# Kernel optimization log

Hardware: AMD Instinct MI355X
Metric: run time of the kernel (lower is better)

## Reference

```python
import jax, jax.numpy as jnp
import numpy as np
from jax import lax

B, C, T = 512, 63, 250          # batch, EEG channels, timepoints
S = 10                           # number of subjects
E = 4                            # emb_size of CNN projection
HID, PROJ = 184, 1024            # hidden_dim (=4*46), embed_dim
EPS = 1e-5
DN = ('NCHW', 'OIHW', 'NCHW')


def setup_inputs() -> dict:
    key = jax.random.key(0)
    ks = jax.random.split(key, 16)
    p = {}
    p['x'] = jax.random.normal(ks[0], (B, C, T), dtype=jnp.float32)
    p['subjects'] = jax.random.randint(ks[1], (B,), 0, S, dtype=jnp.int32)
    # per-subject Linear(T, T): weight [S, T, T], bias [S, T]
    p['W_subj'] = jax.random.normal(ks[2], (S, T, T), dtype=jnp.float32) * 0.02
    p['b_subj'] = jnp.zeros((S, T), dtype=jnp.float32)
    # tsconv
    p['conv1_w'] = jax.random.normal(ks[3], (40, 1, 1, 5), dtype=jnp.float32) * 0.1
    p['conv1_b'] = jnp.zeros((40,), dtype=jnp.float32)
    p['bn1_g'] = jnp.ones((40,), dtype=jnp.float32)
    p['bn1_b'] = jnp.zeros((40,), dtype=jnp.float32)
    p['conv2_w'] = jax.random.normal(ks[4], (40, 40, C, 1), dtype=jnp.float32) * 0.02
    p['conv2_b'] = jnp.zeros((40,), dtype=jnp.float32)
    p['bn2_g'] = jnp.ones((40,), dtype=jnp.float32)
    p['bn2_b'] = jnp.zeros((40,), dtype=jnp.float32)
    # 1x1 projection conv to emb_size
    p['proj_w'] = jax.random.normal(ks[5], (E, 40, 1, 1), dtype=jnp.float32) * 0.1
    p['proj_b'] = jnp.zeros((E,), dtype=jnp.float32)
    # MLP projector
    p['fc1_w'] = jax.random.normal(ks[6], (PROJ, HID), dtype=jnp.float32) * 0.05
    p['fc1_b'] = jnp.zeros((PROJ,), dtype=jnp.float32)
    p['fc2_w'] = jax.random.normal(ks[7], (PROJ, PROJ), dtype=jnp.float32) * 0.02
    p['fc2_b'] = jnp.zeros((PROJ,), dtype=jnp.float32)
    p['ln_g'] = jnp.ones((PROJ,), dtype=jnp.float32)
    p['ln_b'] = jnp.zeros((PROJ,), dtype=jnp.float32)
    return p


def _bn(h, g, b):
    # BatchNorm2d with batch statistics over (N, H, W), NCHW layout
    mu = jnp.mean(h, axis=(0, 2, 3), keepdims=True)
    var = jnp.var(h, axis=(0, 2, 3), keepdims=True)
    return (h - mu) * lax.rsqrt(var + EPS) * g[None, :, None, None] + b[None, :, None, None]


def _avgpool_w(h, k, s):
    # average pool over last (W) dim, kernel k stride s
    summed = lax.reduce_window(h, 0.0, lax.add, (1, 1, 1, k), (1, 1, 1, s), 'VALID')
    return summed / k


def reference(x, subjects, W_subj, b_subj, conv1_w, conv1_b, bn1_g, bn1_b,
              conv2_w, conv2_b, bn2_g, bn2_b, proj_w, proj_b,
              fc1_w, fc1_b, fc2_w, fc2_b, ln_g, ln_b):
    # --- subject-conditioned linear dispatch (grouped GEMM via gather) ---
    Wg = W_subj[subjects]                      # [B, T, T]
    bg = b_subj[subjects]                      # [B, T]
    x_eeg = jnp.einsum('bct,bst->bcs', x, Wg) + bg[:, None, :]   # [B, C, T]

    # --- Spatio_Temporal_CNN ---
    h = x_eeg[:, None, :, :]                   # [B, 1, C, T]
    h = lax.conv_general_dilated(h, conv1_w, (1, 1), 'VALID', dimension_numbers=DN)
    h = h + conv1_b[None, :, None, None]       # [B, 40, C, 246]
    h = _avgpool_w(h, 17, 5)                   # [B, 40, C, 46]
    h = jax.nn.elu(_bn(h, bn1_g, bn1_b))
    h = lax.conv_general_dilated(h, conv2_w, (1, 1), 'VALID', dimension_numbers=DN)
    h = h + conv2_b[None, :, None, None]       # [B, 40, 1, 46]
    h = jax.nn.elu(_bn(h, bn2_g, bn2_b))       # dropout = identity (eval)
    h = lax.conv_general_dilated(h, proj_w, (1, 1), 'VALID', dimension_numbers=DN)
    h = h + proj_b[None, :, None, None]        # [B, E, 1, 46]
    # Rearrange 'b e h w -> b (h w) e' then flatten -> [B, 46*E] = [B, 184]
    z = jnp.transpose(h, (0, 2, 3, 1)).reshape(h.shape[0], -1)

    # --- MLP projector ---
    h1 = z @ fc1_w.T + fc1_b                   # [B, 1024]
    r = jax.nn.gelu(h1, approximate=False) @ fc2_w.T + fc2_b
    h2 = h1 + r                                # ResidualAdd (dropout = identity)
    mu = jnp.mean(h2, axis=-1, keepdims=True)
    var = jnp.var(h2, axis=-1, keepdims=True)
    return (h2 - mu) * lax.rsqrt(var + EPS) * ln_g + ln_b
```

## Files before the change

### kernel.cpp

```cpp
#include <hip/hip_runtime.h>
#include <hip/hip_bf16.h>

#define K2 2520
#define PROJ 1024
#define HID 184
#define N1F (512.f*63.f*46.f)
#define N2F (512.f*46.f)

typedef float f32x4 __attribute__((ext_vector_type(4)));
typedef short bf16x8 __attribute__((ext_vector_type(8)));
typedef unsigned short u16;
typedef unsigned short ushort8 __attribute__((ext_vector_type(8)));
typedef unsigned int u32;
typedef unsigned int u32x2 __attribute__((ext_vector_type(2)));
typedef unsigned int u32x4 __attribute__((ext_vector_type(4)));

__device__ __forceinline__ u16 f2bf(float f) {
    unsigned u = __builtin_bit_cast(unsigned, f);
    return (u16)((u + 0x7FFFu + ((u >> 16) & 1u)) >> 16);
}
__device__ __forceinline__ float bf2f(u16 h) {
    unsigned u = ((unsigned)h) << 16;
    return __builtin_bit_cast(float, u);
}
__device__ __forceinline__ u32 cvtpk(float lo, float hi) {
    u32 r;
    asm("v_cvt_pk_bf16_f32 %0, %1, %2" : "=v"(r) : "v"(lo), "v"(hi));
    return r;
}

__global__ void kX(const float* __restrict__ W, const float* __restrict__ w2,
                   const float* __restrict__ fw1, const float* __restrict__ fw2,
                   u16* __restrict__ Wbf, u16* __restrict__ Wbf2,
                   u16* __restrict__ fwbf1, u16* __restrict__ fwbf2, float* stats) {
    int bid = blockIdx.x, tid = threadIdx.x;
    if (bid == 0 && tid < 320) stats[tid] = 0.f;
    if (bid < 2560) {
        int i = bid*256 + tid;
        int j  = i & 7, kg = (i >> 3) & 3, row = (i >> 5) & 15;
        int nf = (i >> 9) & 15, ks = (i >> 13) & 7, sj = i >> 16;
        int s_ = nf*16 + row, t_ = ks*32 + kg*8 + j;
        float v = (s_ < 250 && t_ < 250) ? W[(size_t)sj*62500 + s_*250 + t_] : 0.f;
        Wbf[i] = f2bf(v);
    } else if (bid < 3034) {
        int i = (bid-2560)*256 + tid;
        int n = i / 2528, k = i - n*2528;
        float v = 0.f;
        if (n < 40 && k < K2) { int c = k/40, o = k - c*40; v = w2[n*K2 + o*63 + c]; }
        Wbf2[i] = f2bf(v);
    } else if (bid < 3802) {
        int i = (bid-3034)*256 + tid;
        int n = i/192, k = i - n*192;
        fwbf1[i] = f2bf(k < HID ? fw1[n*HID + k] : 0.f);
    } else {
        int i = (bid-3802)*256 + tid;
        fwbf2[i] = f2bf(fw2[i]);
    }
}

#define XS(c,s) xs[(c)*258 + (s)]
__global__ __launch_bounds__(256) void kAB(const float* __restrict__ x,
                                           const int* __restrict__ subj,
                                           const u16* __restrict__ Wpk,
                                           const float* __restrict__ bsub,
                                           const float* __restrict__ w1,
                                           const float* __restrict__ b1,
                                           u16* __restrict__ pooled,
                                           float* __restrict__ stats) {
    __shared__ float xs[32*258 + 16];
    __shared__ u16 effh[48*32] __attribute__((aligned(16)));
    __shared__ u16 effl[48*32] __attribute__((aligned(16)));
    __shared__ float biasL[256];
    __shared__ float sS[4][48], sQ[4][48];
    int b = blockIdx.x, ch = blockIdx.y;
    int sj = subj[b];
    int tid = threadIdx.x;
    int wv = tid >> 6, lane = tid & 63, row = lane & 15, kg = lane >> 4;

    {
        int srow = tid >> 3, st8 = tid & 7;
        int cg0 = ch*32 + srow;
        const float* xrow = x + ((size_t)b*63 + (cg0 < 63 ? cg0 : 62))*250;
        #pragma unroll
        for (int q = 0; q < 16; ++q) {
            int c2i = st8 + 8*q;
            if (c2i < 125) {
                float2 v = *(const float2*)&xrow[2*c2i];
                *(float2*)&XS(srow, 2*c2i) = v;
            }
        }
        XS(srow, 250 + st8) = 0.f;
        if (tid < 16) xs[32*258 + tid] = 0.f;
    }
    biasL[tid] = (tid < 250) ? bsub[sj*250 + tid] : 0.f;
    for (int i = tid; i < 1536; i += 256) {
        int o = i >> 5, tap = i & 31;
        float e = 0.f;
        if (o < 40 && tap < 21) {
            #pragma unroll
            for (int k = 0; k < 5; ++k) { int u = tap - k; if (u >= 0 && u <= 16) e += w1[o*5+k]; }
            e *= (1.f/17.f);
        }
        u16 h = f2bf(e);
        effh[i] = h;
        effl[i] = f2bf(e - bf2f(h));
    }
    __syncthreads();

    int cgrp = wv & 1, nfh = wv >> 1;
    const u16* Wp = Wpk + (size_t)sj*65536 + ((size_t)row*4 + kg)*8;
    f32x4 acc[8];
    #pragma unroll
    for (int i = 0; i < 8; ++i) acc[i] = (f32x4){0.f,0.f,0.f,0.f};
    #pragma unroll
    for (int ks = 0; ks < 8; ++ks) {
        int tb = ks*32 + kg*8;
        float av[8];
        #pragma unroll
        for (int j = 0; j < 8; ++j) av[j] = XS(cgrp*16 + row, tb + j);
        u32x4 p;
        p[0]=cvtpk(av[0],av[1]); p[1]=cvtpk(av[2],av[3]);
        p[2]=cvtpk(av[4],av[5]); p[3]=cvtpk(av[6],av[7]);
        bf16x8 af = __builtin_bit_cast(bf16x8, p);
        #pragma unroll
        for (int nf2 = 0; nf2 < 8; ++nf2) {
            bf16x8 bv = *(const bf16x8*)(Wp + (size_t)(ks*16 + nfh*8 + nf2)*512);
            acc[nf2] = __builtin_amdgcn_mfma_f32_16x16x32_bf16(af, bv, acc[nf2], 0, 0, 0);
        }
    }
    __syncthreads();
    int cw = cgrp*16 + kg*4;
    #pragma unroll
    for (int nf2 = 0; nf2 < 8; ++nf2) {
        int s = (nfh*8 + nf2)*16 + row;
        float bias = biasL[s];
        #pragma unroll
        for (int r = 0; r < 4; ++r) XS(cw + r, s) = acc[nf2][r] + bias;
    }
    __syncthreads();

    bf16x8 avh[3], avl[3];
    f32x4 cin3[3];
    #pragma unroll
    for (int nt = 0; nt < 3; ++nt) {
        avh[nt] = *(const bf16x8*)(effh + (nt*16 + row)*32 + kg*8);
        avl[nt] = *(const bf16x8*)(effl + (nt*16 + row)*32 + kg*8);
        int ob = nt*16 + kg*4;
        if (ob < 40) cin3[nt] = *(const f32x4*)&b1[ob];
        else         cin3[nt] = (f32x4){0.f,0.f,0.f,0.f};
    }
    float ss[3][4] = {}, sq[3][4] = {};
    int climit = ch ? 31 : 32;
    for (int c2 = wv; c2 < climit; c2 += 4) {
        u16* prow = pooled + (size_t)b*115920 + (size_t)(ch*32 + c2)*1840;
        #pragma unroll
        for (int mt = 0; mt < 3; ++mt) {
            int base = c2*258 + 5*(mt*16 + row) + kg*8;
            float av[8];
            #pragma unroll
            for (int j = 0; j < 8; ++j) av[j] = xs[base + j];
            u32x4 ph, pl;
            #pragma unroll
            for (int p = 0; p < 4; ++p) {
                u32 h = cvtpk(av[2*p], av[2*p+1]);
                float h0 = __builtin_bit_cast(float, h << 16);
                float h1 = __builtin_bit_cast(float, h & 0xFFFF0000u);
                ph[p] = h;
                pl[p] = cvtpk(av[2*p] - h0, av[2*p+1] - h1);
            }
            bf16x8 bfh = __builtin_bit_cast(bf16x8, ph);
            bf16x8 bfl = __builtin_bit_cast(bf16x8, pl);
            int w = mt*16 + row;
            bool wvalid = w < 46;
            #pragma unroll
            for (int nt = 0; nt < 3; ++nt) {
                f32x4 a = cin3[nt];
                a = __builtin_amdgcn_mfma_f32_16x16x32_bf16(avh[nt], bfl, a, 0, 0, 0);
                a = __builtin_amdgcn_mfma_f32_16x16x32_bf16(avl[nt], bfh, a, 0, 0, 0);
                a = __builtin_amdgcn_mfma_f32_16x16x32_bf16(avh[nt], bfh, a, 0, 0, 0);
                int ob = nt*16 + kg*4;
                if (wvalid && ob < 40) {
                    u32x2 pk;
                    pk[0] = cvtpk(a[0], a[1]);
                    pk[1] = cvtpk(a[2], a[3]);
                    *(u32x2*)&prow[(size_t)w*40 + ob] = pk;
                    #pragma unroll
                    for (int r = 0; r < 4; ++r) {
                        ss[nt][r] += a[r];
                        sq[nt][r] = fmaf(a[r], a[r], sq[nt][r]);
                    }
                }
            }
        }
    }
    #pragma unroll
    for (int nt = 0; nt < 3; ++nt) {
        #pragma unroll
        for (int r = 0; r < 4; ++r) {
            float s = ss[nt][r], q = sq[nt][r];
            s += __shfl_xor(s, 1); q += __shfl_xor(q, 1);
            s += __shfl_xor(s, 2); q += __shfl_xor(q, 2);
            s += __shfl_xor(s, 4); q += __shfl_xor(q, 4);
            s += __shfl_xor(s, 8); q += __shfl_xor(q, 8);
            if (row == 0) {
                int ob = nt*16 + kg*4;
                if (ob < 40) { sS[wv][ob + r] = s; sQ[wv][ob + r] = q; }
            }
        }
    }
    __syncthreads();
    if (tid < 40) {
        float s = sS[0][tid]+sS[1][tid]+sS[2][tid]+sS[3][tid];
        float q = sQ[0][tid]+sQ[1][tid]+sQ[2][tid]+sQ[3][tid];
        atomicAdd(&stats[tid], s);
        atomicAdd(&stats[40 + tid], q);
    }
}

__global__ __launch_bounds__(256) void kD(const u16* __restrict__ pooled,
                                          const u16* __restrict__ Wbf2,
                                          const float* __restrict__ b2,
                                          const float* __restrict__ g1,
                                          const float* __restrict__ bb1,
                                          const float* __restrict__ stats,
                                          float* __restrict__ out2,
                                          float* __restrict__ statw) {
    __shared__ float2 scsh[40];
    __shared__ float mrg[2][64][12];
    __shared__ float redS[2][48], redQ[2][48];
    int tid = threadIdx.x;
    if (tid < 40) {
        float mean = stats[tid] / N1F;
        float var  = stats[40 + tid] / N1F - mean * mean;
        float sc   = g1[tid] * rsqrtf(var + 1e-5f);
        scsh[tid] = make_float2(sc, bb1[tid] - mean * sc);
    }
    __syncthreads();
    int wv = tid >> 6, lane = tid & 63, row = lane & 15, kg = lane >> 4;
    int rowgrp = wv >> 1, khalf = wv & 1;
    int mbase = blockIdx.x*32 + rowgrp*16;
    int m = mbase + row;
    int bb = m / 46, ww = m - bb*46;
    const u16* prl = pooled + (size_t)bb*115920 + (size_t)ww*40;
    f32x4 acc[3];
    #pragma unroll
    for (int i = 0; i < 3; ++i) acc[i] = (f32x4){0.f,0.f,0.f,0.f};

    int ksBeg = khalf ? 39 : 0, ksEnd = khalf ? 79 : 39;
    int t0 = 4*ksBeg + kg;
    int ci = (t0*52429) >> 18, o5i = t0 - 5*ci;
    ushort8 cur = *(const ushort8*)(prl + ci*1840 + o5i*8);
    for (int ks = ksBeg; ks < ksEnd; ++ks) {
        ushort8 nxt = cur;
        if (ks + 1 < ksEnd) {
            int tn = 4*(ks+1) + kg;
            int cn = (tn*52429) >> 18, o5n = tn - 5*cn;
            nxt = *(const ushort8*)(prl + cn*1840 + o5n*8);
        }
        int kbase = ks*32 + kg*8;
        bf16x8 bv0 = *(const bf16x8*)(Wbf2 + (size_t)(row     )*2528 + kbase);
        bf16x8 bv1 = *(const bf16x8*)(Wbf2 + (size_t)(16 + row)*2528 + kbase);
        bf16x8 bv2 = *(const bf16x8*)(Wbf2 + (size_t)(32 + row)*2528 + kbase);
        bf16x8 af;
        bool valid = (ks < 78) | (kg < 3);
        if (valid) {
            int tt = 4*ks + kg;
            int cc = (tt*52429) >> 18;
            int o0 = (tt - 5*cc) * 8;
            #pragma unroll
            for (int j = 0; j < 8; ++j) {
                float2 sshf = scsh[o0 + j];
                float a = fmaf(bf2f(cur[j]), sshf.x, sshf.y);
                float e = a > 0.f ? a : __expf(a) - 1.f;
                af[j] = (short)f2bf(e);
            }
        } else {
            #pragma unroll
            for (int j = 0; j < 8; ++j) af[j] = 0;
        }
        acc[0] = __builtin_amdgcn_mfma_f32_16x16x32_bf16(af, bv0, acc[0], 0, 0, 0);
        acc[1] = __builtin_amdgcn_mfma_f32_16x16x32_bf16(af, bv1, acc[1], 0, 0, 0);
        acc[2] = __builtin_amdgcn_mfma_f32_16x16x32_bf16(af, bv2, acc[2], 0, 0, 0);
        cur = nxt;
    }

    if (khalf) {
        #pragma unroll
        for (int nf = 0; nf < 3; ++nf)
            #pragma unroll
            for (int r = 0; r < 4; ++r) mrg[rowgrp][lane][nf*4 + r] = acc[nf][r];
    }
    __syncthreads();
    if (!khalf) {
        float sN[3] = {0.f,0.f,0.f}, qN[3] = {0.f,0.f,0.f};
        #pragma unroll
        for (int nf = 0; nf < 3; ++nf) {
            int n = nf*16 + row;
            #pragma unroll
            for (int r = 0; r < 4; ++r) acc[nf][r] += mrg[rowgrp][lane][nf*4 + r];
            if (n < 40) {
                float bias = b2[n];
                #pragma unroll
                for (int r = 0; r < 4; ++r) {
                    float v = acc[nf][r] + bias;
                    out2[(size_t)(mbase + kg*4 + r)*40 + n] = v;
                    sN[nf] += v; qN[nf] += v*v;
                }
            }
        }
        #pragma unroll
        for (int nf = 0; nf < 3; ++nf) {
            float s = sN[nf], q = qN[nf];
            s += __shfl_xor(s, 16); q += __shfl_xor(q, 16);
            s += __shfl_xor(s, 32); q += __shfl_xor(q, 32);
            if (kg == 0) { redS[rowgrp][nf*16 + row] = s; redQ[rowgrp][nf*16 + row] = q; }
        }
    }
    __syncthreads();
    if (tid < 40) {
        atomicAdd(&statw[160 + tid], redS[0][tid] + redS[1][tid]);
        atomicAdd(&statw[200 + tid], redQ[0][tid] + redQ[1][tid]);
    }
}

__global__ void kF(const float* __restrict__ out2, const float* __restrict__ stats,
                   const float* __restrict__ g2, const float* __restrict__ bb2,
                   const float* __restrict__ pw, const float* __restrict__ pb,
                   u16* __restrict__ zbf) {
    int b = blockIdx.x, t = threadIdx.x;
    __shared__ float sc[40], sh[40], pws[160];
    __shared__ float o2[1840];
    if (t < 40) {
        float mean = stats[160 + t] / N2F;
        float var  = stats[200 + t] / N2F - mean * mean;
        float s    = g2[t] * rsqrtf(var + 1e-5f);
        sc[t] = s;
        sh[t] = bb2[t] - mean * s;
    }
    if (t < 160) pws[t] = pw[t];
    for (int i = t; i < 1840; i += 256) o2[i] = out2[(size_t)b*1840 + i];
    __syncthreads();
    if (t < 192) {
        float accv = 0.f;
        if (t < HID) {
            int w = t >> 2, e = t & 3;
            accv = pb[e];
            for (int o = 0; o < 40; ++o) {
                float a = o2[w*40 + o];
                float act = a * sc[o] + sh[o];
                act = act > 0.f ? act : __expf(act) - 1.f;
                accv = fmaf(act, pws[e*40 + o], accv);
            }
        }
        zbf[(size_t)b*192 + t] = f2bf(accv);
    }
}

__global__ __launch_bounds__(256) void kG1(const u16* __restrict__ zbf, const u16* __restrict__ fwbf1,
                                           const float* __restrict__ fb,
                                           float* __restrict__ h1, u16* __restrict__ gbf) {
    int n0 = blockIdx.x * 64, m0 = blockIdx.y * 16;
    int tid = threadIdx.x, wv = tid >> 6, lane = tid & 63, row = lane & 15, kg = lane >> 4;
    const u16* zr = zbf + (size_t)(m0 + row) * 192;
    const u16* wr = fwbf1 + (size_t)(n0 + wv*16 + row) * 192;
    f32x4 acc = (f32x4){0.f,0.f,0.f,0.f};
    #pragma unroll
    for (int ks = 0; ks < 6; ++ks) {
        bf16x8 av = *(const bf16x8*)(zr + ks*32 + kg*8);
        bf16x8 bv = *(const bf16x8*)(wr + ks*32 + kg*8);
        acc = __builtin_amdgcn_mfma_f32_16x16x32_bf16(av, bv, acc, 0, 0, 0);
    }
    int n = n0 + wv*16 + row;
    float bias = fb[n];
    #pragma unroll
    for (int r = 0; r < 4; ++r) {
        int m = m0 + kg*4 + r;
        float v = acc[r] + bias;
        h1[(size_t)m*PROJ + n] = v;
        float ge = 0.5f * v * (1.f + erff(v * 0.70710678118f));
        gbf[(size_t)m*PROJ + n] = f2bf(ge);
    }
}

__global__ __launch_bounds__(256) void kG2(const u16* __restrict__ gbf, const u16* __restrict__ fwbf,
                                           const float* __restrict__ fb, const float* __restrict__ h1,
                                           float* __restrict__ h2) {
    int n0 = blockIdx.x * 32, m0 = blockIdx.y * 64;
    int tid = threadIdx.x;
    int wv = tid >> 6, lane = tid & 63, row = lane & 15, kg = lane >> 4;
    const u16* gr = gbf + (size_t)(m0 + wv*16 + row) * PROJ;
    f32x4 acc[2];
    #pragma unroll
    for (int i = 0; i < 2; ++i) acc[i] = (f32x4){0.f,0.f,0.f,0.f};
    for (int ks = 0; ks < 32; ++ks) {
        int kbase = ks*32 + kg*8;
        bf16x8 av  = *(const bf16x8*)(gr + kbase);
        bf16x8 bv0 = *(const bf16x8*)(fwbf + (size_t)(n0      + row)*PROJ + kbase);
        bf16x8 bv1 = *(const bf16x8*)(fwbf + (size_t)(n0 + 16 + row)*PROJ + kbase);
        acc[0] = __builtin_amdgcn_mfma_f32_16x16x32_bf16(av, bv0, acc[0], 0, 0, 0);
        acc[1] = __builtin_amdgcn_mfma_f32_16x16x32_bf16(av, bv1, acc[1], 0, 0, 0);
    }
    int m = m0 + wv*16 + kg*4;
    #pragma unroll
    for (int nf = 0; nf < 2; ++nf) {
        int n = n0 + nf*16 + row;
        float bias = fb[n];
        #pragma unroll
        for (int r = 0; r < 4; ++r)
            h2[(size_t)(m + r)*PROJ + n] = acc[nf][r] + bias + h1[(size_t)(m + r)*PROJ + n];
    }
}

__global__ __launch_bounds__(256) void kG3(const float* __restrict__ h2, const float* __restrict__ lg,
                                           const float* __restrict__ lb, float* __restrict__ out) {
    int b = blockIdx.x, tid = threadIdx.x;
    float4 v = *(const float4*)&h2[(size_t)b*PROJ + tid*4];
    float s = v.x + v.y + v.z + v.w;
    float q = v.x*v.x + v.y*v.y + v.z*v.z + v.w*v.w;
    __shared__ float ps[4], pq[4], mb[2];
    int wave = tid >> 6, lane = tid & 63;
    #pragma unroll
    for (int d = 32; d >= 1; d >>= 1) { s += __shfl_down(s, d); q += __shfl_down(q, d); }
    if (lane == 0) { ps[wave] = s; pq[wave] = q; }
    __syncthreads();
    if (tid == 0) {
        float S = ps[0]+ps[1]+ps[2]+ps[3], Q = pq[0]+pq[1]+pq[2]+pq[3];
        float mean = S / 1024.f, var = Q / 1024.f - mean*mean;
        mb[0] = mean; mb[1] = rsqrtf(var + 1e-5f);
    }
    __syncthreads();
    float mean = mb[0], inv = mb[1];
    float4 g4 = *(const float4*)&lg[tid*4];
    float4 b4 = *(const float4*)&lb[tid*4];
    float4 o4;
    o4.x = (v.x - mean)*inv*g4.x + b4.x;
    o4.y = (v.y - mean)*inv*g4.y + b4.y;
    o4.z = (v.z - mean)*inv*g4.z + b4.z;
    o4.w = (v.w - mean)*inv*g4.w + b4.w;
    *(float4*)&out[(size_t)b*PROJ + tid*4] = o4;
}

extern "C" void kernel_launch(void* const* d_in, const int* in_sizes, int n_in,
                              void* d_out, int out_size, void* d_ws, size_t ws_size,
                              hipStream_t stream) {
    const float* x       = (const float*)d_in[0];
    const int*   subjects= (const int*)  d_in[1];
    const float* W_subj  = (const float*)d_in[2];
    const float* b_subj  = (const float*)d_in[3];
    const float* conv1_w = (const float*)d_in[4];
    const float* conv1_b = (const float*)d_in[5];
    const float* bn1_g   = (const float*)d_in[6];
    const float* bn1_b   = (const float*)d_in[7];
    const float* conv2_w = (const float*)d_in[8];
    const float* conv2_b = (const float*)d_in[9];
    const float* bn2_g   = (const float*)d_in[10];
    const float* bn2_b   = (const float*)d_in[11];
    const float* proj_w  = (const float*)d_in[12];
    const float* proj_b  = (const float*)d_in[13];
    const float* fc1_w   = (const float*)d_in[14];
    const float* fc1_b   = (const float*)d_in[15];
    const float* fc2_w   = (const float*)d_in[16];
    const float* fc2_b   = (const float*)d_in[17];
    const float* ln_g    = (const float*)d_in[18];
    const float* ln_b    = (const float*)d_in[19];
    float* out = (float*)d_out;

    char* ws = (char*)d_ws;
    u16*   pooled = (u16*)  ws;
    float* out2   = (float*)(ws + 118702144);
    u16*   zbf    = (u16*)  (ws + 122470464);
    float* h1     = (float*)(ws + 122667072);
    float* h2     = (float*)(ws + 124764224);
    u16*   gbf    = (u16*)  (ws + 126861376);
    float* stats  = (float*)(ws + 127909952);
    u16*   Wbf    = (u16*)  (ws + 127914048);
    u16*   Wbf2   = (u16*)  (ws + 129224768);
    u16*   fwbf2  = (u16*)  (ws + 129467456);
    u16*   fwbf1  = (u16*)  (ws + 131564608);

    kX  <<<7898, 256, 0, stream>>>(W_subj, conv2_w, fc1_w, fc2_w, Wbf, Wbf2, fwbf1, fwbf2, stats);
    kAB <<<dim3(512, 2), 256, 0, stream>>>(x, subjects, Wbf, b_subj, conv1_w, conv1_b, pooled, stats);
    kD  <<<736, 256, 0, stream>>>(pooled, Wbf2, conv2_b, bn1_g, bn1_b, stats, out2, stats);
    kF  <<<512, 256, 0, stream>>>(out2, stats, bn2_g, bn2_b, proj_w, proj_b, zbf);
    kG1 <<<dim3(16, 32), 256, 0, stream>>>(zbf, fwbf1, fc1_b, h1, gbf);
    kG2 <<<dim3(32, 8), 256, 0, stream>>>(gbf, fwbf2, fc2_b, h1, h2);
    kG3 <<<512, 256, 0, stream>>>(h2, ln_g, ln_b, out);
    (void)in_sizes; (void)n_in; (void)out_size; (void)ws_size;
}
```

Before: 254.0 us.

## Split kAB into 16-channel blocks and kD into 4-way K-split

kAB now handles 16 channels per block, so each block stages half as much input in shared memory and the grid doubles to 512x4 blocks. kD processes 16 output rows per block, with the K dimension split four ways across waves and the partial sums merged through shared memory; its grid doubles to 1472 blocks. The ELU output in kD is also packed into bf16 with cvtpk instead of per-element conversion. The goal is more blocks and less LDS per block for better occupancy and latency hiding. The cost is more redundant per-block setup (eff weights, bias loads, stats atomics) and extra merge traffic.

```diff
diff --git a/kernel.cpp b/kernel.cpp
--- a/kernel.cpp
+++ b/kernel.cpp
@@ -67,7 +67,7 @@
                                            const float* __restrict__ b1,
                                            u16* __restrict__ pooled,
                                            float* __restrict__ stats) {
-    __shared__ float xs[32*258 + 16];
+    __shared__ float xs[16*258 + 16];
     __shared__ u16 effh[48*32] __attribute__((aligned(16)));
     __shared__ u16 effl[48*32] __attribute__((aligned(16)));
     __shared__ float biasL[256];
@@ -78,19 +78,19 @@
     int wv = tid >> 6, lane = tid & 63, row = lane & 15, kg = lane >> 4;
 
     {
-        int srow = tid >> 3, st8 = tid & 7;
-        int cg0 = ch*32 + srow;
+        int srow = tid >> 4, st16 = tid & 15;
+        int cg0 = ch*16 + srow;
         const float* xrow = x + ((size_t)b*63 + (cg0 < 63 ? cg0 : 62))*250;
         #pragma unroll
-        for (int q = 0; q < 16; ++q) {
-            int c2i = st8 + 8*q;
+        for (int q = 0; q < 8; ++q) {
+            int c2i = st16 + 16*q;
             if (c2i < 125) {
                 float2 v = *(const float2*)&xrow[2*c2i];
                 *(float2*)&XS(srow, 2*c2i) = v;
             }
         }
-        XS(srow, 250 + st8) = 0.f;
-        if (tid < 16) xs[32*258 + tid] = 0.f;
+        if (st16 < 8) XS(srow, 250 + st16) = 0.f;
+        if (tid < 16) xs[16*258 + tid] = 0.f;
     }
     biasL[tid] = (tid < 250) ? bsub[sj*250 + tid] : 0.f;
     for (int i = tid; i < 1536; i += 256) {
@@ -107,32 +107,31 @@
     }
     __syncthreads();
 
-    int cgrp = wv & 1, nfh = wv >> 1;
     const u16* Wp = Wpk + (size_t)sj*65536 + ((size_t)row*4 + kg)*8;
-    f32x4 acc[8];
-    #pragma unroll
-    for (int i = 0; i < 8; ++i) acc[i] = (f32x4){0.f,0.f,0.f,0.f};
+    f32x4 acc[4];
+    #pragma unroll
+    for (int i = 0; i < 4; ++i) acc[i] = (f32x4){0.f,0.f,0.f,0.f};
     #pragma unroll
     for (int ks = 0; ks < 8; ++ks) {
         int tb = ks*32 + kg*8;
         float av[8];
         #pragma unroll
-        for (int j = 0; j < 8; ++j) av[j] = XS(cgrp*16 + row, tb + j);
+        for (int j = 0; j < 8; ++j) av[j] = XS(row, tb + j);
         u32x4 p;
         p[0]=cvtpk(av[0],av[1]); p[1]=cvtpk(av[2],av[3]);
         p[2]=cvtpk(av[4],av[5]); p[3]=cvtpk(av[6],av[7]);
         bf16x8 af = __builtin_bit_cast(bf16x8, p);
         #pragma unroll
-        for (int nf2 = 0; nf2 < 8; ++nf2) {
-            bf16x8 bv = *(const bf16x8*)(Wp + (size_t)(ks*16 + nfh*8 + nf2)*512);
+        for (int nf2 = 0; nf2 < 4; ++nf2) {
+            bf16x8 bv = *(const bf16x8*)(Wp + (size_t)(ks*16 + wv*4 + nf2)*512);
             acc[nf2] = __builtin_amdgcn_mfma_f32_16x16x32_bf16(af, bv, acc[nf2], 0, 0, 0);
         }
     }
     __syncthreads();
-    int cw = cgrp*16 + kg*4;
-    #pragma unroll
-    for (int nf2 = 0; nf2 < 8; ++nf2) {
-        int s = (nfh*8 + nf2)*16 + row;
+    int cw = kg*4;
+    #pragma unroll
+    for (int nf2 = 0; nf2 < 4; ++nf2) {
+        int s = (wv*4 + nf2)*16 + row;
         float bias = biasL[s];
         #pragma unroll
         for (int r = 0; r < 4; ++r) XS(cw + r, s) = acc[nf2][r] + bias;
@@ -150,9 +149,9 @@
         else         cin3[nt] = (f32x4){0.f,0.f,0.f,0.f};
     }
     float ss[3][4] = {}, sq[3][4] = {};
-    int climit = ch ? 31 : 32;
+    int climit = (ch == 3) ? 15 : 16;
     for (int c2 = wv; c2 < climit; c2 += 4) {
-        u16* prow = pooled + (size_t)b*115920 + (size_t)(ch*32 + c2)*1840;
+        u16* prow = pooled + (size_t)b*115920 + (size_t)(ch*16 + c2)*1840;
         #pragma unroll
         for (int mt = 0; mt < 3; ++mt) {
             int base = c2*258 + 5*(mt*16 + row) + kg*8;
@@ -226,8 +225,8 @@
                                           float* __restrict__ out2,
                                           float* __restrict__ statw) {
     __shared__ float2 scsh[40];
-    __shared__ float mrg[2][64][12];
-    __shared__ float redS[2][48], redQ[2][48];
+    __shared__ float mrg[3][64][12];
+    __shared__ float redS[48], redQ[48];
     int tid = threadIdx.x;
     if (tid < 40) {
         float mean = stats[tid] / N1F;
@@ -237,8 +236,7 @@
     }
     __syncthreads();
     int wv = tid >> 6, lane = tid & 63, row = lane & 15, kg = lane >> 4;
-    int rowgrp = wv >> 1, khalf = wv & 1;
-    int mbase = blockIdx.x*32 + rowgrp*16;
+    int mbase = blockIdx.x*16;
     int m = mbase + row;
     int bb = m / 46, ww = m - bb*46;
     const u16* prl = pooled + (size_t)bb*115920 + (size_t)ww*40;
@@ -246,7 +244,7 @@
     #pragma unroll
     for (int i = 0; i < 3; ++i) acc[i] = (f32x4){0.f,0.f,0.f,0.f};
 
-    int ksBeg = khalf ? 39 : 0, ksEnd = khalf ? 79 : 39;
+    int ksBeg = 20*wv, ksEnd = (wv == 3) ? 79 : 20*(wv+1);
     int t0 = 4*ksBeg + kg;
     int ci = (t0*52429) >> 18, o5i = t0 - 5*ci;
     ushort8 cur = *(const ushort8*)(prl + ci*1840 + o5i*8);
@@ -267,13 +265,17 @@
             int tt = 4*ks + kg;
             int cc = (tt*52429) >> 18;
             int o0 = (tt - 5*cc) * 8;
+            float e[8];
             #pragma unroll
             for (int j = 0; j < 8; ++j) {
                 float2 sshf = scsh[o0 + j];
                 float a = fmaf(bf2f(cur[j]), sshf.x, sshf.y);
-                float e = a > 0.f ? a : __expf(a) - 1.f;
-                af[j] = (short)f2bf(e);
-            }
+                e[j] = a > 0.f ? a : __expf(a) - 1.f;
+            }
+            u32x4 pk;
+            #pragma unroll
+            for (int p = 0; p < 4; ++p) pk[p] = cvtpk(e[2*p], e[2*p+1]);
+            af = __builtin_bit_cast(bf16x8, pk);
         } else {
             #pragma unroll
             for (int j = 0; j < 8; ++j) af[j] = 0;
@@ -284,20 +286,21 @@
         cur = nxt;
     }
 
-    if (khalf) {
+    if (wv) {
         #pragma unroll
         for (int nf = 0; nf < 3; ++nf)
             #pragma unroll
-            for (int r = 0; r < 4; ++r) mrg[rowgrp][lane][nf*4 + r] = acc[nf][r];
-    }
-    __syncthreads();
-    if (!khalf) {
+            for (int r = 0; r < 4; ++r) mrg[wv-1][lane][nf*4 + r] = acc[nf][r];
+    }
+    __syncthreads();
+    if (wv == 0) {
         float sN[3] = {0.f,0.f,0.f}, qN[3] = {0.f,0.f,0.f};
         #pragma unroll
         for (int nf = 0; nf < 3; ++nf) {
             int n = nf*16 + row;
             #pragma unroll
-            for (int r = 0; r < 4; ++r) acc[nf][r] += mrg[rowgrp][lane][nf*4 + r];
+            for (int r = 0; r < 4; ++r)
+                acc[nf][r] += mrg[0][lane][nf*4+r] + mrg[1][lane][nf*4+r] + mrg[2][lane][nf*4+r];
             if (n < 40) {
                 float bias = b2[n];
                 #pragma unroll
@@ -313,13 +316,16 @@
             float s = sN[nf], q = qN[nf];
             s += __shfl_xor(s, 16); q += __shfl_xor(q, 16);
             s += __shfl_xor(s, 32); q += __shfl_xor(q, 32);
-            if (kg == 0) { redS[rowgrp][nf*16 + row] = s; redQ[rowgrp][nf*16 + row] = q; }
+            if (kg == 0) {
+                int n = nf*16 + row;
+                if (n < 48) { redS[n] = s; redQ[n] = q; }
+            }
         }
     }
     __syncthreads();
     if (tid < 40) {
-        atomicAdd(&statw[160 + tid], redS[0][tid] + redS[1][tid]);
-        atomicAdd(&statw[200 + tid], redQ[0][tid] + redQ[1][tid]);
+        atomicAdd(&statw[160 + tid], redS[tid]);
+        atomicAdd(&statw[200 + tid], redQ[tid]);
     }
 }
 
@@ -479,8 +485,8 @@
     u16*   fwbf1  = (u16*)  (ws + 131564608);
 
     kX  <<<7898, 256, 0, stream>>>(W_subj, conv2_w, fc1_w, fc2_w, Wbf, Wbf2, fwbf1, fwbf2, stats);
-    kAB <<<dim3(512, 2), 256, 0, stream>>>(x, subjects, Wbf, b_subj, conv1_w, conv1_b, pooled, stats);
-    kD  <<<736, 256, 0, stream>>>(pooled, Wbf2, conv2_b, bn1_g, bn1_b, stats, out2, stats);
+    kAB <<<dim3(512, 4), 256, 0, stream>>>(x, subjects, Wbf, b_subj, conv1_w, conv1_b, pooled, stats);
+    kD  <<<1472, 256, 0, stream>>>(pooled, Wbf2, conv2_b, bn1_g, bn1_b, stats, out2, stats);
     kF  <<<512, 256, 0, stream>>>(out2, stats, bn2_g, bn2_b, proj_w, proj_b, zbf);
     kG1 <<<dim3(16, 32), 256, 0, stream>>>(zbf, fwbf1, fc1_b, h1, gbf);
     kG2 <<<dim3(32, 8), 256, 0, stream>>>(gbf, fwbf2, fc2_b, h1, h2);
```

New measurement: 289.0 us. +13.8%, slower.
